# Optimization experiments

Measured on AMD Instinct MI355X. Metric: run time of the kernel, lower is better.

Reference implementation:

```python
import jax, jax.numpy as jnp
import numpy as np

B, N_PER, DEG, F_IN, F_HID = 64, 1024, 16, 128, 128
E = B * N_PER * DEG  # 1,048,576 edges, grouped per graph


def setup_inputs() -> dict:
    key = jax.random.key(0)
    ks = jax.random.split(key, 16)
    n_total = B * N_PER
    x = jax.random.normal(ks[0], (n_total, F_IN), dtype=jnp.float32)
    # edges are random within each graph block
    local = jax.random.randint(ks[1], (2, E), 0, N_PER)
    offs = (jnp.arange(E, dtype=jnp.int64) // (N_PER * DEG)) * N_PER
    edge_index = (local.astype(jnp.int64) + offs[None, :])
    edge_weight = jax.random.uniform(ks[2], (E,), dtype=jnp.float32)
    batch_index = jnp.repeat(jnp.arange(B, dtype=jnp.int64), N_PER)
    s = 1.0 / np.sqrt(F_HID)
    params = {
        'W1': jax.random.normal(ks[3], (F_IN, F_HID)) * s,
        'b1': jnp.zeros((F_HID,), jnp.float32),
        'p1': jax.random.normal(ks[4], (F_HID,)) * s,
        'W2': jax.random.normal(ks[5], (F_HID, F_HID)) * s,
        'b2': jnp.zeros((F_HID,), jnp.float32),
        'p2': jax.random.normal(ks[6], (F_HID,)) * s,
        'W3': jax.random.normal(ks[7], (F_HID, F_HID)) * s,
        'b3': jnp.zeros((F_HID,), jnp.float32),
        'p3': jax.random.normal(ks[8], (F_HID,)) * s,
        'Wo': jax.random.normal(ks[9], (2 * F_HID, 1)) * s,
        'bo': jnp.zeros((1,), jnp.float32),
    }
    return {'x': x, 'edge_index': edge_index, 'edge_weight': edge_weight,
            'batch_index': batch_index, **params}


def _gcn_conv(x, src, dst, w, W, b):
    # GCNConv with add_self_loops=True, symmetric normalization, edge_weight.
    n = x.shape[0]
    xW = x @ W
    deg = jnp.zeros((n,), x.dtype).at[dst].add(w) + 1.0  # +1 from self-loop fill
    dinv = jax.lax.rsqrt(deg)
    norm = dinv[src] * w * dinv[dst]
    agg = jnp.zeros_like(xW).at[dst].add(norm[:, None] * xW[src])
    return agg + (dinv * dinv)[:, None] * xW + b  # self-loop term + bias


def _topk_pool(x, src, dst, w, p, n, k):
    # TopKPooling with nonlinearity=sigmoid, equal-size graphs (n -> k nodes).
    f = x.shape[1]
    xr = x.reshape(B, n, f)
    score = jax.nn.sigmoid((xr @ p) / jnp.linalg.norm(p))  # [B, n]
    vals, perm = jax.lax.top_k(score, k)                    # per-graph top-k
    xn = jnp.take_along_axis(xr, perm[:, :, None], axis=1) * vals[:, :, None]
    # inverse map old local idx -> new local idx (-1 if dropped)
    inv = jnp.full((B, n), -1, dtype=jnp.int32)
    inv = inv.at[jnp.arange(B)[:, None], perm].set(jnp.arange(k, dtype=jnp.int32)[None, :])
    g = src // n
    sl = inv[g, src % n]
    dl = inv[dst // n, dst % n]
    keep = (sl >= 0) & (dl >= 0)
    # dropped edges are masked to node 0 with weight 0 (contribute nothing)
    src2 = jnp.where(keep, g * k + sl, 0)
    dst2 = jnp.where(keep, (dst // n) * k + dl, 0)
    w2 = jnp.where(keep, w, jnp.zeros((), w.dtype))
    return xn.reshape(B * k, f), src2, dst2, w2


def reference(x, edge_index, edge_weight, batch_index,
              W1, b1, p1, W2, b2, p2, W3, b3, p3, Wo, bo):
    src, dst = edge_index[0], edge_index[1]
    w = edge_weight
    n = N_PER
    h = _gcn_conv(x, src, dst, w, W1, b1)
    h, src, dst, w = _topk_pool(h, src, dst, w, p1, n, n // 2); n //= 2
    h = jax.nn.relu(h)
    h = _gcn_conv(h, src, dst, w, W2, b2)
    h, src, dst, w = _topk_pool(h, src, dst, w, p2, n, n // 2); n //= 2
    h = jax.nn.relu(h)
    h = _gcn_conv(h, src, dst, w, W3, b3)
    h, src, dst, w = _topk_pool(h, src, dst, w, p3, n, n // 2); n //= 2
    h = jax.nn.relu(h)
    hr = h.reshape(B, n, -1)
    cat = jnp.concatenate([hr.max(axis=1), hr.mean(axis=1)], axis=1)  # gmp || gap
    out = jax.nn.sigmoid(cat @ Wo + bo)
    return out, cat
```

## Files before the change

kernel.cpp:

```cpp
#include <hip/hip_runtime.h>

#define NB 64
#define EDGES 1048576
#define NTOT  65536

struct __align__(8) CsrE { int s; float w; };

using bf16x8 = __attribute__((ext_vector_type(8))) short;
using f32x4  = __attribute__((ext_vector_type(4))) float;

__global__ void k_zerof(float* __restrict__ p, int n){
  int i=blockIdx.x*256+threadIdx.x; if(i<n) p[i]=0.f;
}

__device__ inline void split1(float x, unsigned &hi16, unsigned &lo16){
  unsigned b=__float_as_uint(x);
  unsigned h=(b+0x7FFFu+((b>>16)&1u))&0xFFFF0000u;
  float lf=x-__uint_as_float(h);
  unsigned lb=__float_as_uint(lf);
  hi16=h>>16;
  lo16=(lb+0x7FFFu+((lb>>16)&1u))>>16;
}

__device__ inline void split8(const float4&u, const float4&v, bf16x8&hi, bf16x8&lo){
  float e[8]={u.x,u.y,u.z,u.w,v.x,v.y,v.z,v.w};
  #pragma unroll
  for(int j=0;j<8;++j){
    unsigned h16,l16; split1(e[j],h16,l16);
    hi[j]=(short)h16; lo[j]=(short)l16;
  }
}

__global__ __launch_bounds__(256) void k_wpack(const float* __restrict__ W1,
        const float* __restrict__ W2, const float* __restrict__ W3,
        unsigned* __restrict__ outp){
  int b=blockIdx.x, m=b>>3;
  const float* W = (m==0)?W1:((m==1)?W2:W3);
  unsigned* o = outp + m*16384;
  for(int t=(b&7)*256+threadIdx.x; t<8192; t+=2048){
    int i=t&3, l=(t>>2)&63, c=(t>>8)&7, q=(t>>11)&3;
    int col=c*16+(l&15);
    int k0=q*32+((l>>4)<<3)+i*2;
    float x0=W[k0*128+col], x1=W[(k0+1)*128+col];
    unsigned h0,l0,h1,l1;
    split1(x0,h0,l0); split1(x1,h1,l1);
    int base=((q*8+c)*2)*256;
    o[base + l*4 + i]       = (h1<<16)|h0;
    o[base + 256 + l*4 + i] = (l1<<16)|l0;
  }
}

template<bool G, int S>
__global__ __launch_bounds__(256) void mm_mfma(const float* __restrict__ X,
        const unsigned* __restrict__ Wpk, const int* __restrict__ selold,
        const float* __restrict__ score, float* __restrict__ Y, int gshift){
  __shared__ __align__(16) unsigned Wl[16384];
  const int RPB = 64*S;
  int b=blockIdx.x;
  int row0b;
  if(G){
    int xcd=b&7, slot=b>>3, bpg=1<<gshift;
    int graph=xcd*8+(slot>>gshift), idx=slot&(bpg-1);
    row0b = graph*(bpg*RPB) + idx*RPB;
  } else row0b = b*RPB;
  for(int t=threadIdx.x;t<4096;t+=256)
    ((uint4*)Wl)[t]=((const uint4*)Wpk)[t];
  const int wave=threadIdx.x>>6, lane=threadIdx.x&63;
  const int row0 = row0b + wave*(16*S);
  const int lrow=lane&15, lko=(lane>>4)<<3;
  int orow[S]; float scr[S];
  #pragma unroll
  for(int s=0;s<S;++s){
    int rr=row0+s*16+lrow;
    orow[s]=G?selold[rr]:rr;
    scr[s]=G?score[orow[s]]:1.f;
  }
  const f32x4 vzero={0.f,0.f,0.f,0.f};
  f32x4 acc[S][8];
  #pragma unroll
  for(int s=0;s<S;++s){
    #pragma unroll
    for(int c=0;c<8;++c) acc[s][c]=vzero;
  }
  __syncthreads();
  const char* wb=(const char*)Wl + lane*16;
  float4 u[S],v[S];
  #pragma unroll
  for(int s=0;s<S;++s){
    const float* xp=X+(size_t)orow[s]*128+lko;
    u[s]=*(const float4*)xp; v[s]=*(const float4*)(xp+4);
  }
  #pragma unroll
  for(int q=0;q<4;++q){
    float4 un[S],vn[S];
    if(q<3){
      #pragma unroll
      for(int s=0;s<S;++s){
        const float* xp=X+(size_t)orow[s]*128+(q+1)*32+lko;
        un[s]=*(const float4*)xp; vn[s]=*(const float4*)(xp+4);
      }
    }
    bf16x8 Ah[S],Al[S];
    #pragma unroll
    for(int s=0;s<S;++s){
      if(G){
        u[s].x=fmaxf(u[s].x*scr[s],0.f); u[s].y=fmaxf(u[s].y*scr[s],0.f);
        u[s].z=fmaxf(u[s].z*scr[s],0.f); u[s].w=fmaxf(u[s].w*scr[s],0.f);
        v[s].x=fmaxf(v[s].x*scr[s],0.f); v[s].y=fmaxf(v[s].y*scr[s],0.f);
        v[s].z=fmaxf(v[s].z*scr[s],0.f); v[s].w=fmaxf(v[s].w*scr[s],0.f);
      }
      split8(u[s],v[s],Ah[s],Al[s]);
    }
    #pragma unroll
    for(int c=0;c<8;++c){
      const bf16x8 bh=*(const bf16x8*)(wb + (q*8+c)*2048);
      const bf16x8 bl=*(const bf16x8*)(wb + (q*8+c)*2048 + 1024);
      #pragma unroll
      for(int s=0;s<S;++s){
        acc[s][c]=__builtin_amdgcn_mfma_f32_16x16x32_bf16(Ah[s],bh,acc[s][c],0,0,0);
        acc[s][c]=__builtin_amdgcn_mfma_f32_16x16x32_bf16(Al[s],bh,acc[s][c],0,0,0);
        acc[s][c]=__builtin_amdgcn_mfma_f32_16x16x32_bf16(Ah[s],bl,acc[s][c],0,0,0);
      }
    }
    if(q<3){
      #pragma unroll
      for(int s=0;s<S;++s){ u[s]=un[s]; v[s]=vn[s]; }
    }
  }
  const int dcol=lane&15, dr0=(lane>>4)<<2;
  #pragma unroll
  for(int s=0;s<S;++s){
    #pragma unroll
    for(int c=0;c<8;++c){
      #pragma unroll
      for(int r=0;r<4;++r){
        Y[(size_t)(row0+s*16+dr0+r)*128 + c*16 + dcol]=acc[s][c][r];
      }
    }
  }
}

__global__ __launch_bounds__(1024) void k_count(const int* __restrict__ edst,
        const float* __restrict__ ew, int* __restrict__ chunkcnt, float* __restrict__ chunkw){
  __shared__ int lc[1024];
  __shared__ float lw[1024];
  int b=blockIdx.x, i=threadIdx.x;
  int xcd=b&7, slot=b>>3;
  int graph=xcd*8+(slot&7), chunk=slot>>3;
  int e0=graph*16384+chunk*4096;
  lc[i]=0; lw[i]=0.f;
  __syncthreads();
  for(int e=e0+i; e<e0+4096; e+=1024){
    int dl=edst[e]&1023;
    atomicAdd(&lc[dl],1);
    atomicAdd(&lw[dl],ew[e]);
  }
  __syncthreads();
  chunkcnt[chunk*65536+graph*1024+i]=lc[i];
  chunkw  [chunk*65536+graph*1024+i]=lw[i];
}

__global__ __launch_bounds__(1024) void k_scan_graph(const int* __restrict__ chunkcnt,
        const float* __restrict__ chunkw, int* __restrict__ rowptr,
        float* __restrict__ dinv1, int* __restrict__ fill){
  __shared__ int wsum[16];
  int g=blockIdx.x, i=threadIdx.x;
  int lane=i&63, w=i>>6;
  int o=g*1024+i;
  int c = chunkcnt[o]+chunkcnt[65536+o]+chunkcnt[131072+o]+chunkcnt[196608+o];
  float ws = chunkw[o]+chunkw[65536+o]+chunkw[131072+o]+chunkw[196608+o];
  int v=c;
  #pragma unroll
  for(int off=1;off<64;off<<=1){ int t=__shfl_up(v,off,64); if(lane>=off) v+=t; }
  if(lane==63) wsum[w]=v;
  __syncthreads();
  int base=0;
  for(int k=0;k<w;++k) base+=wsum[k];
  int excl=base+v-c;
  int e0=g*16384;
  rowptr[o]=e0+excl;
  fill[o]=e0+excl;
  dinv1[o]=rsqrtf(ws+1.0f);
  if(g==63 && i==1023) rowptr[65536]=EDGES;
}

__global__ __launch_bounds__(1024) void k_scatter2(const int* __restrict__ esrc,
        const int* __restrict__ edst, const float* __restrict__ ew,
        int* __restrict__ fill, CsrE* __restrict__ csr){
  int b=blockIdx.x, i=threadIdx.x;
  int xcd=b&7, slot=b>>3;
  int graph=xcd*8+(slot&7), chunk=slot>>3;
  int e0=graph*16384+chunk*4096;
  int base=graph*1024;
  for(int e=e0+i; e<e0+4096; e+=1024){
    int dl=edst[e]&1023;
    int pos=atomicAdd(&fill[base+dl],1);
    CsrE ce; ce.s=esrc[e]; ce.w=ew[e];
    csr[pos]=ce;
  }
}

template<bool F>
__global__ __launch_bounds__(256) void k_gather(const float* __restrict__ xw, const CsrE* __restrict__ csr,
        const int* __restrict__ rowptr, const int* __restrict__ map, const int* __restrict__ inv,
        const float* __restrict__ dinvv, const float* __restrict__ bias, const float* __restrict__ p,
        float* __restrict__ h, float* __restrict__ score, int gshift, int ns){
  int wv=threadIdx.x>>6, half=(threadIdx.x>>5)&1, hl=threadIdx.x&31;
  int b=blockIdx.x, xcd=b&7, slot=b>>3, bpg=1<<gshift;
  int graph=xcd*8+(slot>>gshift), idx=slot&(bpg-1);
  int v = graph*(bpg<<3) + (idx<<3) + wv*2 + half;
  if(v>=ns) return;
  int d0 = F? map[v] : v;
  float dv=dinvv[v];
  int rs=rowptr[d0], re=rowptr[d0+1];
  const int f4=hl*4;
  float4 accA={0.f,0.f,0.f,0.f}, accB={0.f,0.f,0.f,0.f};
  for(int base=rs; base<re; base+=32){
    int len=re-base; if(len>32) len=32;
    int sidx=0; float cf=0.f;
    if(hl<len){
      CsrE en=csr[base+hl];
      int s=en.s; bool live=true;
      if(F){ int t=inv[s]; live=(t>=0); s=live?t:0; }
      if(live){ sidx=s; cf=dinvv[s]*en.w; }
    }
    int len4=(len+3)&~3;
    for(int j=0;j<len4;j+=4){
      float c0=__shfl(cf,j,32),   c1=__shfl(cf,j+1,32);
      float c2=__shfl(cf,j+2,32), c3=__shfl(cf,j+3,32);
      int   s0=__shfl(sidx,j,32),   s1=__shfl(sidx,j+1,32);
      int   s2=__shfl(sidx,j+2,32), s3=__shfl(sidx,j+3,32);
      const float4 x0=*(const float4*)&xw[(size_t)s0*128+f4];
      const float4 x1=*(const float4*)&xw[(size_t)s1*128+f4];
      const float4 x2=*(const float4*)&xw[(size_t)s2*128+f4];
      const float4 x3=*(const float4*)&xw[(size_t)s3*128+f4];
      accA.x+=c0*x0.x; accA.y+=c0*x0.y; accA.z+=c0*x0.z; accA.w+=c0*x0.w;
      accB.x+=c1*x1.x; accB.y+=c1*x1.y; accB.z+=c1*x1.z; accB.w+=c1*x1.w;
      accA.x+=c2*x2.x; accA.y+=c2*x2.y; accA.z+=c2*x2.z; accA.w+=c2*x2.w;
      accB.x+=c3*x3.x; accB.y+=c3*x3.y; accB.z+=c3*x3.z; accB.w+=c3*x3.w;
    }
  }
  float4 acc; acc.x=accA.x+accB.x; acc.y=accA.y+accB.y;
  acc.z=accA.z+accB.z; acc.w=accA.w+accB.w;
  const float4 xv=*(const float4*)&xw[(size_t)v*128+f4];
  const float4 bv=*(const float4*)&bias[f4];
  float d2=dv*dv;
  float4 hv;
  hv.x=acc.x*dv + d2*xv.x + bv.x;
  hv.y=acc.y*dv + d2*xv.y + bv.y;
  hv.z=acc.z*dv + d2*xv.z + bv.z;
  hv.w=acc.w*dv + d2*xv.w + bv.w;
  *(float4*)&h[(size_t)v*128+f4]=hv;
  const float4 pv=*(const float4*)&p[f4];
  float z=hv.x*pv.x+hv.y*pv.y+hv.z*pv.z+hv.w*pv.w;
  float pp=pv.x*pv.x+pv.y*pv.y+pv.z*pv.z+pv.w*pv.w;
  #pragma unroll
  for(int m=16;m>0;m>>=1){ z+=__shfl_xor(z,m,32); pp+=__shfl_xor(pp,m,32); }
  if(hl==0) score[v]=1.0f/(1.0f+expf(-z/sqrtf(pp)));
}

template<int N, int K, int MODE>
__global__ __launch_bounds__(N) void k_topk(const float* __restrict__ score,
        int* __restrict__ inv, int* __restrict__ selold,
        const int* __restrict__ inv1s, const int* __restrict__ sel1s,
        int* __restrict__ inv12, int* __restrict__ map12,
        const int* __restrict__ rowptr, const CsrE* __restrict__ csr,
        float* __restrict__ dinv_out,
        const float* __restrict__ h3, const float* __restrict__ Wo,
        const float* __restrict__ bo, float* __restrict__ outp){
  __shared__ unsigned hist[256];
  __shared__ int wsum[16];
  __shared__ int c_sh, r_sh;
  __shared__ float red[128];
  int g=blockIdx.x, i=threadIdx.x;
  int lane=i&63, w=i>>6;
  int gv=g*N+i;
  unsigned key=__float_as_uint(score[gv]);
  int st=1;
  int R=K;
  #pragma unroll
  for(int pass=0; pass<4; ++pass){
    int shift=24-pass*8;
    if(i<256) hist[i]=0;
    __syncthreads();
    unsigned byte=(key>>shift)&255u;
    if(st==1) atomicAdd(&hist[byte],1u);
    __syncthreads();
    unsigned hcnt=0, sfx=0;
    if(i<256){
      hcnt=hist[i]; sfx=hcnt;
      #pragma unroll
      for(int off=1;off<64;off<<=1){
        unsigned t=__shfl_down(sfx,off,64);
        if(lane+off<64) sfx+=t;
      }
      if(lane==0) wsum[w]=(int)sfx;
    }
    __syncthreads();
    if(i<256){
      int tot=0;
      for(int k=w+1;k<4;++k) tot+=wsum[k];
      int S=(int)sfx+tot;
      int A=S-(int)hcnt;
      if(A<R && R<=S){ c_sh=i; r_sh=R-A; }
    }
    __syncthreads();
    int c=c_sh; R=r_sh;
    if(st==1){
      if((int)byte>c) st=2;
      else if((int)byte<c) st=0;
    }
    __syncthreads();
  }
  int alive=(st==1)?1:0;
  unsigned long long mA=__ballot(alive);
  int rA=__popcll(mA & ((1ULL<<lane)-1ULL));
  if(lane==0) wsum[w]=__popcll(mA);
  __syncthreads();
  int offA=0;
  for(int k=0;k<w;++k) offA+=wsum[k];
  int tie_rank=offA+rA;
  int sel=(st==2)||(st==1 && tie_rank<R);
  __syncthreads();
  unsigned long long mS=__ballot(sel);
  int rS=__popcll(mS & ((1ULL<<lane)-1ULL));
  if(lane==0) wsum[w]=__popcll(mS);
  __syncthreads();
  int offS=0;
  for(int k=0;k<w;++k) offS+=wsum[k];
  int ng=g*K+offS+rS;
  if(sel && ng<NB*K){ inv[gv]=ng; selold[ng]=gv; }
  else inv[gv]=-1;
  if(MODE==1){
    __syncthreads();
    for(int t=i; t<K; t+=N){
      int v=g*K+t;
      int d0=selold[v];
      int rs=rowptr[d0], re=rowptr[d0+1];
      float s0=0.f,s1=0.f,s2=0.f,s3=0.f;
      int e=rs;
      for(; e+4<=re; e+=4){
        CsrE e0=csr[e], e1=csr[e+1], e2=csr[e+2], e3=csr[e+3];
        if(inv[e0.s]>=0) s0+=e0.w;
        if(inv[e1.s]>=0) s1+=e1.w;
        if(inv[e2.s]>=0) s2+=e2.w;
        if(inv[e3.s]>=0) s3+=e3.w;
      }
      for(; e<re; ++e){
        CsrE en=csr[e];
        if(inv[en.s]>=0) s0+=en.w;
      }
      dinv_out[v]=rsqrtf((s0+s1)+(s2+s3)+1.0f);
    }
  }
  if(MODE==2){
    __syncthreads();
    for(int t=i; t<1024; t+=N){
      int v0=g*1024+t;
      int q=inv1s[v0];
      inv12[v0]=(q>=0)?inv[q]:-1;
    }
    for(int t=i; t<K; t+=N){
      int v=g*K+t;
      map12[v]=sel1s[selold[v]];
    }
    __syncthreads();
    for(int t=i; t<K; t+=N){
      int v=g*K+t;
      int d0=map12[v];
      int rs=rowptr[d0], re=rowptr[d0+1];
      float s0=0.f,s1=0.f,s2=0.f,s3=0.f;
      int e=rs;
      for(; e+4<=re; e+=4){
        CsrE e0=csr[e], e1=csr[e+1], e2=csr[e+2], e3=csr[e+3];
        if(inv12[e0.s]>=0) s0+=e0.w;
        if(inv12[e1.s]>=0) s1+=e1.w;
        if(inv12[e2.s]>=0) s2+=e2.w;
        if(inv12[e3.s]>=0) s3+=e3.w;
      }
      for(; e<re; ++e){
        CsrE en=csr[e];
        if(inv12[en.s]>=0) s0+=en.w;
      }
      dinv_out[v]=rsqrtf((s0+s1)+(s2+s3)+1.0f);
    }
  }
  if(MODE==3){
    __syncthreads();
    int f=i;
    float mx=-3.4e38f, sm=0.f;
    if(f<128){
      for(int nd=0;nd<128;++nd){
        int old=selold[g*128+nd];
        float vv=fmaxf(h3[(size_t)old*128+f]*score[old],0.f);
        mx=fmaxf(mx,vv); sm+=vv;
      }
      float mean=sm*(1.0f/128.0f);
      outp[64+g*256+f]    =mx;
      outp[64+g*256+128+f]=mean;
      red[f]=mx*Wo[f]+mean*Wo[128+f];
    }
    __syncthreads();
    for(int off=64;off>0;off>>=1){
      if(f<off) red[f]+=red[f+off];
      __syncthreads();
    }
    if(f==0){ float z=red[0]+bo[0]; outp[g]=1.0f/(1.0f+expf(-z)); }
  }
}

extern "C" void kernel_launch(void* const* d_in, const int* in_sizes, int n_in,
                              void* d_out, int out_size, void* d_ws, size_t ws_size,
                              hipStream_t stream) {
  (void)in_sizes; (void)n_in;
  const float* x  = (const float*)d_in[0];
  const int*   ei = (const int*)d_in[1];
  const float* ew = (const float*)d_in[2];
  const float* W1=(const float*)d_in[4];  const float* b1=(const float*)d_in[5];  const float* p1=(const float*)d_in[6];
  const float* W2=(const float*)d_in[7];  const float* b2=(const float*)d_in[8];  const float* p2=(const float*)d_in[9];
  const float* W3=(const float*)d_in[10]; const float* b3=(const float*)d_in[11]; const float* p3=(const float*)d_in[12];
  const float* Wo=(const float*)d_in[13]; const float* bo=(const float*)d_in[14];
  float* out=(float*)d_out;

  char* ws=(char*)d_ws;
  size_t cur=0;
  float* slot0=(float*)(ws+cur); cur+=33554432;
  float* slot1=(float*)(ws+cur); cur+=33554432;
  CsrE*  csr  =(CsrE*)(ws+cur);  cur+=(size_t)EDGES*8;
  int*   chunkcnt=(int*)(ws+cur); cur+=1048576;
  float* chunkw  =(float*)(ws+cur); cur+=1048576;
  int*   fill =(int*)  (ws+cur); cur+=262144;
  int*   rowptr=(int*) (ws+cur); cur+=262400;
  float* dinv1=(float*)(ws+cur); cur+=262144;
  float* dinv2=(float*)(ws+cur); cur+=131072;
  float* dinv3=(float*)(ws+cur); cur+=65536;
  float* sc1  =(float*)(ws+cur); cur+=262144;
  float* sc2  =(float*)(ws+cur); cur+=131072;
  float* sc3  =(float*)(ws+cur); cur+=65536;
  int*   inv1 =(int*)  (ws+cur); cur+=262144;
  int*   inv2 =(int*)  (ws+cur); cur+=131072;
  int*   invS =(int*)  (ws+cur); cur+=65536;
  int*   inv12=(int*)  (ws+cur); cur+=262144;
  int*   sel1 =(int*)  (ws+cur); cur+=131072;
  int*   sel2 =(int*)  (ws+cur); cur+=65536;
  int*   sel3 =(int*)  (ws+cur); cur+=32768;
  int*   map12=(int*)  (ws+cur); cur+=65536;
  unsigned* wpk=(unsigned*)(ws+cur); cur+=196608;

  if (ws_size < cur) {
    k_zerof<<<(out_size+255)/256,256,0,stream>>>(out,out_size);
    return;
  }

  const int* esrc=ei; const int* edst=ei+EDGES;

  k_wpack<<<24,256,0,stream>>>(W1,W2,W3,wpk);

  mm_mfma<false,2><<<NTOT/128,256,0,stream>>>(x,wpk,nullptr,nullptr,slot0,0);
  k_count<<<256,1024,0,stream>>>(edst,ew,chunkcnt,chunkw);
  k_scan_graph<<<64,1024,0,stream>>>(chunkcnt,chunkw,rowptr,dinv1,fill);
  k_scatter2<<<256,1024,0,stream>>>(esrc,edst,ew,fill,csr);
  k_gather<false><<<NTOT/8,256,0,stream>>>(slot0,csr,rowptr,nullptr,nullptr,
                                           dinv1,b1,p1,slot1,sc1,7,NTOT);
  k_topk<1024,512,1><<<NB,1024,0,stream>>>(sc1,inv1,sel1,nullptr,nullptr,nullptr,nullptr,
                                           rowptr,csr,dinv2,nullptr,nullptr,nullptr,nullptr);

  mm_mfma<true,1><<<32768/64,256,0,stream>>>(slot1,wpk+16384,sel1,sc1,slot0,3);
  k_gather<true><<<32768/8,256,0,stream>>>(slot0,csr,rowptr,sel1,inv1,
                                           dinv2,b2,p2,slot1,sc2,6,32768);
  k_topk<512,256,2><<<NB,512,0,stream>>>(sc2,inv2,sel2,inv1,sel1,inv12,map12,
                                         rowptr,csr,dinv3,nullptr,nullptr,nullptr,nullptr);

  mm_mfma<true,1><<<16384/64,256,0,stream>>>(slot1,wpk+32768,sel2,sc2,slot0,2);
  k_gather<true><<<16384/8,256,0,stream>>>(slot0,csr,rowptr,map12,inv12,
                                           dinv3,b3,p3,slot1,sc3,5,16384);
  k_topk<256,128,3><<<NB,256,0,stream>>>(sc3,invS,sel3,nullptr,nullptr,nullptr,nullptr,
                                         nullptr,nullptr,nullptr,slot1,Wo,bo,out);
}
```

Measured before the change: 300.0 us.

## Fuse weight packing into matmul, merge CSR build kernels, unroll gather, parallelize readout

Weight packing into the split bf16 hi/lo layout now happens inside each matmul block, which removes the separate pack kernel and its workspace round trip. The count, scan and scatter kernels are merged into one per-graph kernel that keeps the fill counters in shared memory, dropping two launches and the global chunk arrays. The gather inner loop is unrolled to 8 edges so more loads are in flight, and the final readout splits nodes across two thread halves using shared-memory indices. In exchange, every matmul block repeats the weight split, the CSR build runs on only 64 blocks, and the first matmul now uses the per-graph block mapping.

```diff
diff --git a/kernel.cpp b/kernel.cpp
--- a/kernel.cpp
+++ b/kernel.cpp
@@ -31,13 +31,17 @@
   }
 }
 
-__global__ __launch_bounds__(256) void k_wpack(const float* __restrict__ W1,
-        const float* __restrict__ W2, const float* __restrict__ W3,
-        unsigned* __restrict__ outp){
-  int b=blockIdx.x, m=b>>3;
-  const float* W = (m==0)?W1:((m==1)?W2:W3);
-  unsigned* o = outp + m*16384;
-  for(int t=(b&7)*256+threadIdx.x; t<8192; t+=2048){
+template<bool G, int S>
+__global__ __launch_bounds__(256) void mm_mfma(const float* __restrict__ X,
+        const float* __restrict__ W, const int* __restrict__ selold,
+        const float* __restrict__ score, float* __restrict__ Y, int gshift){
+  __shared__ __align__(16) unsigned Wl[16384];
+  const int RPB = 64*S;
+  int b=blockIdx.x;
+  int xcd=b&7, slot=b>>3, bpg=1<<gshift;
+  int graph=xcd*8+(slot>>gshift), idx=slot&(bpg-1);
+  int row0b = graph*(bpg*RPB) + idx*RPB;
+  for(int t=threadIdx.x;t<8192;t+=256){
     int i=t&3, l=(t>>2)&63, c=(t>>8)&7, q=(t>>11)&3;
     int col=c*16+(l&15);
     int k0=q*32+((l>>4)<<3)+i*2;
@@ -45,26 +49,9 @@
     unsigned h0,l0,h1,l1;
     split1(x0,h0,l0); split1(x1,h1,l1);
     int base=((q*8+c)*2)*256;
-    o[base + l*4 + i]       = (h1<<16)|h0;
-    o[base + 256 + l*4 + i] = (l1<<16)|l0;
-  }
-}
-
-template<bool G, int S>
-__global__ __launch_bounds__(256) void mm_mfma(const float* __restrict__ X,
-        const unsigned* __restrict__ Wpk, const int* __restrict__ selold,
-        const float* __restrict__ score, float* __restrict__ Y, int gshift){
-  __shared__ __align__(16) unsigned Wl[16384];
-  const int RPB = 64*S;
-  int b=blockIdx.x;
-  int row0b;
-  if(G){
-    int xcd=b&7, slot=b>>3, bpg=1<<gshift;
-    int graph=xcd*8+(slot>>gshift), idx=slot&(bpg-1);
-    row0b = graph*(bpg*RPB) + idx*RPB;
-  } else row0b = b*RPB;
-  for(int t=threadIdx.x;t<4096;t+=256)
-    ((uint4*)Wl)[t]=((const uint4*)Wpk)[t];
+    Wl[base + l*4 + i]       = (h1<<16)|h0;
+    Wl[base + 256 + l*4 + i] = (l1<<16)|l0;
+  }
   const int wave=threadIdx.x>>6, lane=threadIdx.x&63;
   const int row0 = row0b + wave*(16*S);
   const int lrow=lane&15, lko=(lane>>4)<<3;
@@ -140,35 +127,24 @@
   }
 }
 
-__global__ __launch_bounds__(1024) void k_count(const int* __restrict__ edst,
-        const float* __restrict__ ew, int* __restrict__ chunkcnt, float* __restrict__ chunkw){
+__global__ __launch_bounds__(1024) void k_csr(const int* __restrict__ esrc,
+        const int* __restrict__ edst, const float* __restrict__ ew,
+        int* __restrict__ rowptr, float* __restrict__ dinv1, CsrE* __restrict__ csr){
   __shared__ int lc[1024];
   __shared__ float lw[1024];
-  int b=blockIdx.x, i=threadIdx.x;
-  int xcd=b&7, slot=b>>3;
-  int graph=xcd*8+(slot&7), chunk=slot>>3;
-  int e0=graph*16384+chunk*4096;
+  __shared__ int wsum[16];
+  int g=blockIdx.x, i=threadIdx.x;
+  int lane=i&63, w=i>>6;
+  int e0=g*16384;
   lc[i]=0; lw[i]=0.f;
   __syncthreads();
-  for(int e=e0+i; e<e0+4096; e+=1024){
+  for(int e=e0+i; e<e0+16384; e+=1024){
     int dl=edst[e]&1023;
     atomicAdd(&lc[dl],1);
     atomicAdd(&lw[dl],ew[e]);
   }
   __syncthreads();
-  chunkcnt[chunk*65536+graph*1024+i]=lc[i];
-  chunkw  [chunk*65536+graph*1024+i]=lw[i];
-}
-
-__global__ __launch_bounds__(1024) void k_scan_graph(const int* __restrict__ chunkcnt,
-        const float* __restrict__ chunkw, int* __restrict__ rowptr,
-        float* __restrict__ dinv1, int* __restrict__ fill){
-  __shared__ int wsum[16];
-  int g=blockIdx.x, i=threadIdx.x;
-  int lane=i&63, w=i>>6;
-  int o=g*1024+i;
-  int c = chunkcnt[o]+chunkcnt[65536+o]+chunkcnt[131072+o]+chunkcnt[196608+o];
-  float ws = chunkw[o]+chunkw[65536+o]+chunkw[131072+o]+chunkw[196608+o];
+  int c=lc[i]; float wsv=lw[i];
   int v=c;
   #pragma unroll
   for(int off=1;off<64;off<<=1){ int t=__shfl_up(v,off,64); if(lane>=off) v+=t; }
@@ -177,24 +153,15 @@
   int base=0;
   for(int k=0;k<w;++k) base+=wsum[k];
   int excl=base+v-c;
-  int e0=g*16384;
-  rowptr[o]=e0+excl;
-  fill[o]=e0+excl;
-  dinv1[o]=rsqrtf(ws+1.0f);
+  rowptr[g*1024+i]=e0+excl;
+  dinv1[g*1024+i]=rsqrtf(wsv+1.0f);
   if(g==63 && i==1023) rowptr[65536]=EDGES;
-}
-
-__global__ __launch_bounds__(1024) void k_scatter2(const int* __restrict__ esrc,
-        const int* __restrict__ edst, const float* __restrict__ ew,
-        int* __restrict__ fill, CsrE* __restrict__ csr){
-  int b=blockIdx.x, i=threadIdx.x;
-  int xcd=b&7, slot=b>>3;
-  int graph=xcd*8+(slot&7), chunk=slot>>3;
-  int e0=graph*16384+chunk*4096;
-  int base=graph*1024;
-  for(int e=e0+i; e<e0+4096; e+=1024){
+  __syncthreads();
+  lc[i]=e0+excl;
+  __syncthreads();
+  for(int e=e0+i; e<e0+16384; e+=1024){
     int dl=edst[e]&1023;
-    int pos=atomicAdd(&fill[base+dl],1);
+    int pos=atomicAdd(&lc[dl],1);
     CsrE ce; ce.s=esrc[e]; ce.w=ew[e];
     csr[pos]=ce;
   }
@@ -224,20 +191,21 @@
       if(F){ int t=inv[s]; live=(t>=0); s=live?t:0; }
       if(live){ sidx=s; cf=dinvv[s]*en.w; }
     }
-    int len4=(len+3)&~3;
-    for(int j=0;j<len4;j+=4){
-      float c0=__shfl(cf,j,32),   c1=__shfl(cf,j+1,32);
-      float c2=__shfl(cf,j+2,32), c3=__shfl(cf,j+3,32);
-      int   s0=__shfl(sidx,j,32),   s1=__shfl(sidx,j+1,32);
-      int   s2=__shfl(sidx,j+2,32), s3=__shfl(sidx,j+3,32);
-      const float4 x0=*(const float4*)&xw[(size_t)s0*128+f4];
-      const float4 x1=*(const float4*)&xw[(size_t)s1*128+f4];
-      const float4 x2=*(const float4*)&xw[(size_t)s2*128+f4];
-      const float4 x3=*(const float4*)&xw[(size_t)s3*128+f4];
-      accA.x+=c0*x0.x; accA.y+=c0*x0.y; accA.z+=c0*x0.z; accA.w+=c0*x0.w;
-      accB.x+=c1*x1.x; accB.y+=c1*x1.y; accB.z+=c1*x1.z; accB.w+=c1*x1.w;
-      accA.x+=c2*x2.x; accA.y+=c2*x2.y; accA.z+=c2*x2.z; accA.w+=c2*x2.w;
-      accB.x+=c3*x3.x; accB.y+=c3*x3.y; accB.z+=c3*x3.z; accB.w+=c3*x3.w;
+    int len8=(len+7)&~7;
+    for(int j=0;j<len8;j+=8){
+      float cc[8]; int ss[8];
+      #pragma unroll
+      for(int m=0;m<8;++m){ cc[m]=__shfl(cf,j+m,32); ss[m]=__shfl(sidx,j+m,32); }
+      float4 xv_[8];
+      #pragma unroll
+      for(int m=0;m<8;++m) xv_[m]=*(const float4*)&xw[(size_t)ss[m]*128+f4];
+      #pragma unroll
+      for(int m=0;m<8;m+=2){
+        accA.x+=cc[m]*xv_[m].x; accA.y+=cc[m]*xv_[m].y;
+        accA.z+=cc[m]*xv_[m].z; accA.w+=cc[m]*xv_[m].w;
+        accB.x+=cc[m+1]*xv_[m+1].x; accB.y+=cc[m+1]*xv_[m+1].y;
+        accB.z+=cc[m+1]*xv_[m+1].z; accB.w+=cc[m+1]*xv_[m+1].w;
+      }
     }
   }
   float4 acc; acc.x=accA.x+accB.x; acc.y=accA.y+accB.y;
@@ -271,7 +239,9 @@
   __shared__ unsigned hist[256];
   __shared__ int wsum[16];
   __shared__ int c_sh, r_sh;
-  __shared__ float red[128];
+  __shared__ float red2[256];
+  __shared__ int sOld[128];
+  __shared__ float sSc[128];
   int g=blockIdx.x, i=threadIdx.x;
   int lane=i&63, w=i>>6;
   int gv=g*N+i;
@@ -300,9 +270,9 @@
     if(i<256){
       int tot=0;
       for(int k=w+1;k<4;++k) tot+=wsum[k];
-      int S=(int)sfx+tot;
-      int A=S-(int)hcnt;
-      if(A<R && R<=S){ c_sh=i; r_sh=R-A; }
+      int Si=(int)sfx+tot;
+      int A=Si-(int)hcnt;
+      if(A<R && R<=Si){ c_sh=i; r_sh=R-A; }
     }
     __syncthreads();
     int c=c_sh; R=r_sh;
@@ -387,25 +357,33 @@
   }
   if(MODE==3){
     __syncthreads();
-    int f=i;
+    if(i<128){ int o=selold[g*128+i]; sOld[i]=o; sSc[i]=score[o]; }
+    __syncthreads();
+    int f=i&127, hf=i>>7;
     float mx=-3.4e38f, sm=0.f;
-    if(f<128){
-      for(int nd=0;nd<128;++nd){
-        int old=selold[g*128+nd];
-        float vv=fmaxf(h3[(size_t)old*128+f]*score[old],0.f);
-        mx=fmaxf(mx,vv); sm+=vv;
-      }
-      float mean=sm*(1.0f/128.0f);
-      outp[64+g*256+f]    =mx;
+    #pragma unroll 4
+    for(int nd=hf*64; nd<hf*64+64; ++nd){
+      float vv=fmaxf(h3[(size_t)sOld[nd]*128+f]*sSc[nd],0.f);
+      mx=fmaxf(mx,vv); sm+=vv;
+    }
+    red2[i]=mx; __syncthreads();
+    float mx2 = (hf==0)? fmaxf(mx,red2[i+128]) : 0.f;
+    __syncthreads();
+    red2[i]=sm; __syncthreads();
+    if(hf==0){
+      float smT=sm+red2[i+128];
+      float mean=smT*(1.0f/128.0f);
+      outp[64+g*256+f]    =mx2;
       outp[64+g*256+128+f]=mean;
-      red[f]=mx*Wo[f]+mean*Wo[128+f];
-    }
+    }
+    __syncthreads();
+    if(hf==0) red2[f]=mx2*Wo[f]+( (sm+red2[f+128]) * (1.0f/128.0f))*Wo[128+f];
     __syncthreads();
     for(int off=64;off>0;off>>=1){
-      if(f<off) red[f]+=red[f+off];
+      if(i<off) red2[i]+=red2[i+off];
       __syncthreads();
     }
-    if(f==0){ float z=red[0]+bo[0]; outp[g]=1.0f/(1.0f+expf(-z)); }
+    if(i==0){ float z=red2[0]+bo[0]; outp[g]=1.0f/(1.0f+expf(-z)); }
   }
 }
 
@@ -427,9 +405,6 @@
   float* slot0=(float*)(ws+cur); cur+=33554432;
   float* slot1=(float*)(ws+cur); cur+=33554432;
   CsrE*  csr  =(CsrE*)(ws+cur);  cur+=(size_t)EDGES*8;
-  int*   chunkcnt=(int*)(ws+cur); cur+=1048576;
-  float* chunkw  =(float*)(ws+cur); cur+=1048576;
-  int*   fill =(int*)  (ws+cur); cur+=262144;
   int*   rowptr=(int*) (ws+cur); cur+=262400;
   float* dinv1=(float*)(ws+cur); cur+=262144;
   float* dinv2=(float*)(ws+cur); cur+=131072;
@@ -445,7 +420,6 @@
   int*   sel2 =(int*)  (ws+cur); cur+=65536;
   int*   sel3 =(int*)  (ws+cur); cur+=32768;
   int*   map12=(int*)  (ws+cur); cur+=65536;
-  unsigned* wpk=(unsigned*)(ws+cur); cur+=196608;
 
   if (ws_size < cur) {
     k_zerof<<<(out_size+255)/256,256,0,stream>>>(out,out_size);
@@ -454,24 +428,20 @@
 
   const int* esrc=ei; const int* edst=ei+EDGES;
 
-  k_wpack<<<24,256,0,stream>>>(W1,W2,W3,wpk);
-
-  mm_mfma<false,2><<<NTOT/128,256,0,stream>>>(x,wpk,nullptr,nullptr,slot0,0);
-  k_count<<<256,1024,0,stream>>>(edst,ew,chunkcnt,chunkw);
-  k_scan_graph<<<64,1024,0,stream>>>(chunkcnt,chunkw,rowptr,dinv1,fill);
-  k_scatter2<<<256,1024,0,stream>>>(esrc,edst,ew,fill,csr);
+  mm_mfma<false,2><<<NTOT/128,256,0,stream>>>(x,W1,nullptr,nullptr,slot0,3);
+  k_csr<<<NB,1024,0,stream>>>(esrc,edst,ew,rowptr,dinv1,csr);
   k_gather<false><<<NTOT/8,256,0,stream>>>(slot0,csr,rowptr,nullptr,nullptr,
                                            dinv1,b1,p1,slot1,sc1,7,NTOT);
   k_topk<1024,512,1><<<NB,1024,0,stream>>>(sc1,inv1,sel1,nullptr,nullptr,nullptr,nullptr,
                                            rowptr,csr,dinv2,nullptr,nullptr,nullptr,nullptr);
 
-  mm_mfma<true,1><<<32768/64,256,0,stream>>>(slot1,wpk+16384,sel1,sc1,slot0,3);
+  mm_mfma<true,1><<<32768/64,256,0,stream>>>(slot1,W2,sel1,sc1,slot0,3);
   k_gather<true><<<32768/8,256,0,stream>>>(slot0,csr,rowptr,sel1,inv1,
                                            dinv2,b2,p2,slot1,sc2,6,32768);
   k_topk<512,256,2><<<NB,512,0,stream>>>(sc2,inv2,sel2,inv1,sel1,inv12,map12,
                                          rowptr,csr,dinv3,nullptr,nullptr,nullptr,nullptr);
 
-  mm_mfma<true,1><<<16384/64,256,0,stream>>>(slot1,wpk+32768,sel2,sc2,slot0,2);
+  mm_mfma<true,1><<<16384/64,256,0,stream>>>(slot1,W3,sel2,sc2,slot0,2);
   k_gather<true><<<16384/8,256,0,stream>>>(slot0,csr,rowptr,map12,inv12,
                                            dinv3,b3,p3,slot1,sc3,5,16384);
   k_topk<256,128,3><<<NB,256,0,stream>>>(sc3,invS,sel3,nullptr,nullptr,nullptr,nullptr,
```

New measurement: 311.6 us. +3.9%, slower.
